# Performance work log

Measured on AMD Instinct MI355X. Metric: run time of the kernel, lower is better.

The kernel has to match this reference:

```python
import jax, jax.numpy as jnp
import numpy as np

B = 2
G = 256            # bev grid size per axis at this stride
STRIDE = 2
PAD = 2
EMB = 128
NPF = 64           # num_pos_feats = emb_dim // 2
LR = np.array([-51.2, -51.2, -3.0, 51.2, 51.2, 1.0], np.float32)
VS = np.array([0.2, 0.2], np.float32)
OFFSET = -128      # round(lr_min / (voxel * stride))
SQRT_DIM = float(np.sqrt(EMB))
Q = 65536
V = B * G * G


def pos2posemb2d(pos, num_pos_feats=NPF, temperature=10000.0):
    # standard interleaved sin/cos 2d position embedding (y first, then x)
    pos = pos * (2.0 * np.pi)
    dim_t = jnp.arange(num_pos_feats, dtype=jnp.float32)
    dim_t = temperature ** (2.0 * (dim_t // 2) / num_pos_feats)
    px = pos[..., 0:1] / dim_t
    py = pos[..., 1:2] / dim_t
    px = jnp.stack((jnp.sin(px[..., 0::2]), jnp.cos(px[..., 1::2])), axis=-1).reshape(pos.shape[0], -1)
    py = jnp.stack((jnp.sin(py[..., 0::2]), jnp.cos(py[..., 1::2])), axis=-1).reshape(pos.shape[0], -1)
    return jnp.concatenate((py, px), axis=-1)


def mlp(x, w1, b1, w2, b2):
    return jax.nn.relu(x @ w1 + b1) @ w2 + b2


def setup_inputs():
    key = jax.random.key(0)
    ks = jax.random.split(key, 16)
    # dense BEV grid of value centers -> value_map scatter is collision-free
    idx = jnp.arange(V)
    b = idx // (G * G)
    x = (idx % (G * G)) // G
    y = idx % G
    ctr_coor = jnp.stack([b, (x - 128) * STRIDE, (y - 128) * STRIDE], axis=-1).astype(jnp.int32)
    ctr_feat = jax.random.normal(ks[0], (V, EMB), jnp.float32)
    bq = jax.random.randint(ks[1], (Q,), 0, B).astype(jnp.float32)
    xy = jax.random.uniform(ks[2], (Q, 2), jnp.float32, -51.0, 51.0)
    ref_pts = jnp.concatenate([bq[:, None], xy], axis=1)
    s = 0.02
    p = lambda k, sh: jax.random.normal(k, sh, jnp.float32) * s
    return dict(
        ref_pts=ref_pts, ctr_coor=ctr_coor, ctr_feat=ctr_feat,
        q_w1=p(ks[3], (EMB, 2 * EMB)), q_b1=jnp.zeros((2 * EMB,), jnp.float32),
        q_w2=p(ks[4], (2 * EMB, EMB)), q_b2=jnp.zeros((EMB,), jnp.float32),
        v_w1=p(ks[5], (EMB, 2 * EMB)), v_b1=jnp.zeros((2 * EMB,), jnp.float32),
        v_w2=p(ks[6], (2 * EMB, EMB)), v_b2=jnp.zeros((EMB,), jnp.float32),
        se_wr=p(ks[7], (EMB, EMB)), se_br=jnp.zeros((EMB,), jnp.float32),
        se_we=p(ks[8], (EMB, EMB)), se_be=jnp.zeros((EMB,), jnp.float32),
    )


def _forward(ref_pts, ctr_feat, q_w1, q_b1, q_w2, q_b2, v_w1, v_b1, v_w2, v_b2,
             se_wr, se_br, se_we, se_be, ctr_coor):
    nv = ctr_feat.shape[0]
    lr = jnp.asarray(LR)
    vs = jnp.asarray(VS)
    # indices2metric: voxel center positions in meters
    ctr_xy = (ctr_coor[:, 1:].astype(jnp.float32) + 0.5) * vs
    # coor_to_indices: grid indices at current stride
    ctr_inds = ctr_coor[:, 1:] // STRIDE - OFFSET                 # (V,2) in [0,G)
    ref_coor = jnp.floor(ref_pts[:, 1:] / vs)                     # metric2indices
    ref_inds = (ref_coor / STRIDE - OFFSET).astype(jnp.int32)     # (Q,2) in [0,G)
    # normalized positions in [0,1]
    qp = (ref_pts[:, 1:] - lr[0:2]) / (lr[3:5] - lr[0:2])
    vp = (ctr_xy - lr[0:2]) / (lr[3:5] - lr[0:2])
    qpos = mlp(pos2posemb2d(qp), q_w1, q_b1, q_w2, q_b2)          # (Q,d)
    vpos = mlp(pos2posemb2d(vp), v_w1, v_b1, v_w2, v_b2)          # (V,d)
    # SELayer_Linear: gate value pos-emb by features
    gate = jax.nn.sigmoid(jax.nn.relu(ctr_feat @ se_wr + se_br) @ se_we + se_be)
    vpos = vpos * gate
    # build padded index map and gather 3x3 neighborhoods
    vmap_grid = -jnp.ones((B, G + 2 * PAD, G + 2 * PAD), jnp.int32)
    vmap_grid = vmap_grid.at[ctr_coor[:, 0], ctr_inds[:, 0] + PAD, ctr_inds[:, 1] + PAD].set(
        jnp.arange(nv, dtype=jnp.int32))
    r = jnp.arange(-1, 2)
    nbrs = jnp.stack(jnp.meshgrid(r, r, indexing='ij'), axis=-1).reshape(-1, 2)  # (9,2)
    bq = ref_pts[:, 0].astype(jnp.int32)
    nx = ref_inds[:, 0:1] + PAD + nbrs[:, 0]                      # (Q,9)
    ny = ref_inds[:, 1:2] + PAD + nbrs[:, 1]
    v_idx = vmap_grid[bq[:, None], nx, ny] + 1                    # missing -> 0 (padded zero row)
    vpos_pad = jnp.concatenate([jnp.zeros((1, EMB), vpos.dtype), vpos], axis=0)
    feat_pad = jnp.concatenate([jnp.zeros((1, EMB), ctr_feat.dtype), ctr_feat], axis=0)
    score = jnp.einsum('qd,qnd->qn', qpos, vpos_pad[v_idx]) / SQRT_DIM
    attn = jax.nn.softmax(score, axis=-1)
    return jnp.einsum('qn,qnd->qd', attn, feat_pad[v_idx])       # (Q,d)


def reference(ref_pts, ctr_coor, ctr_feat, q_w1, q_b1, q_w2, q_b2,
              v_w1, v_b1, v_w2, v_b2, se_wr, se_br, se_we, se_be):
    return _forward(ref_pts, ctr_feat, q_w1, q_b1, q_w2, q_b2,
                    v_w1, v_b1, v_w2, v_b2, se_wr, se_br, se_we, se_be, ctr_coor)
```

## Files before the change

### kernel.cpp

```cpp
#include <hip/hip_runtime.h>
#include <math.h>

#define SCALE_INV_SQRT_D 0.08838834764831844f

#define NQ 65536
#define NV 131072
#define NBKT 2048

typedef __attribute__((ext_vector_type(8))) short s16x8;
typedef __attribute__((ext_vector_type(4))) float f32x4;

__device__ __forceinline__ unsigned short f2bf(float f) {
    unsigned int u = __builtin_bit_cast(unsigned int, f);
    u += 0x7fffu + ((u >> 16) & 1u);
    return (unsigned short)(u >> 16);
}
__device__ __forceinline__ float bf2f(unsigned short s) {
    return __builtin_bit_cast(float, (unsigned)s << 16);
}
#define LGKM0() asm volatile("s_waitcnt lgkmcnt(0)" ::: "memory")
#define SBAR0() __builtin_amdgcn_sched_barrier(0)

__device__ __forceinline__ int kperm(int kk) {
    int i = kk & 7, gg = (kk >> 3) & 3, ks = kk >> 5;
    return (ks << 5) + ((i & 4) << 2) + (gg << 2) + (i & 3);
}

__global__ __launch_bounds__(256) void prep_kernel(
    const float* __restrict__ qw1, const float* __restrict__ qw2,
    const float* __restrict__ vw1, const float* __restrict__ vw2,
    const float* __restrict__ sewr, const float* __restrict__ sewe,
    unsigned short* __restrict__ wbuf)
{
    int i = blockIdx.x * 256 + threadIdx.x;
    float v;
    if (i < 32768)        { int li = i;          int n = li >> 7, k = li & 127;          v = qw1[k * 256 + n]; }
    else if (i < 65536)   { int li = i - 32768;  int n = li >> 8, k = kperm(li & 255);   v = qw2[k * 128 + n]; }
    else if (i < 98304)   { int li = i - 65536;  int n = li >> 7, k = li & 127;          v = vw1[k * 256 + n]; }
    else if (i < 131072)  { int li = i - 98304;  int n = li >> 8, k = kperm(li & 255);   v = vw2[k * 128 + n]; }
    else if (i < 147456)  { int li = i - 131072; int n = li >> 7, k = li & 127;          v = sewr[k * 128 + n]; }
    else                  { int li = i - 147456; int n = li >> 7, k = kperm(li & 127);   v = sewe[k * 128 + n]; }
    wbuf[i] = f2bf(v);
}

__global__ __launch_bounds__(256) void sort_zero_kernel(int* __restrict__ counts) {
    counts[blockIdx.x * 256 + threadIdx.x] = 0;
}

__global__ __launch_bounds__(256) void sort_count_kernel(
    const float* __restrict__ ref_pts, int* __restrict__ counts,
    unsigned short* __restrict__ qb)
{
    int qi = blockIdx.x * 256 + threadIdx.x;
    int b = (int)ref_pts[qi * 3 + 0];
    float x = ref_pts[qi * 3 + 1], y = ref_pts[qi * 3 + 2];
    int xi = (int)(floorf(x * 5.0f) * 0.5f + 128.0f);
    int yi = (int)(floorf(y * 5.0f) * 0.5f + 128.0f);
    int bucket = (b << 10) | ((xi >> 3) << 5) | (yi >> 3);
    qb[qi] = (unsigned short)bucket;
    atomicAdd(&counts[bucket], 1);
}

__global__ __launch_bounds__(1024) void sort_scan_kernel(
    const int* __restrict__ counts, int* __restrict__ offs)
{
    __shared__ int a[NBKT], b[NBKT];
    const int t = threadIdx.x;
    int c0 = counts[t], c1 = counts[t + 1024];
    a[t] = c0; a[t + 1024] = c1;
    __syncthreads();
    int* src = a; int* dst = b;
    for (int d = 1; d < NBKT; d <<= 1) {
        dst[t]        = src[t]        + ((t >= d)        ? src[t - d]        : 0);
        dst[t + 1024] = src[t + 1024] + ((t + 1024 >= d) ? src[t + 1024 - d] : 0);
        __syncthreads();
        int* tmp = src; src = dst; dst = tmp;
    }
    offs[t]        = src[t] - c0;
    offs[t + 1024] = src[t + 1024] - c1;
}

__global__ __launch_bounds__(256) void sort_scatter_kernel(
    const unsigned short* __restrict__ qb, int* __restrict__ offs,
    int* __restrict__ perm)
{
    int qi = blockIdx.x * 256 + threadIdx.x;
    int pos = atomicAdd(&offs[qb[qi]], 1);
    perm[pos] = qi;
}

__global__ __launch_bounds__(512, 4) void se_gate_kernel(
    const float* __restrict__ ctr_feat,
    const unsigned short* __restrict__ sewrt,
    const float* __restrict__ sebr,
    const unsigned short* __restrict__ sewetp,
    const float* __restrict__ sebe,
    unsigned short* __restrict__ gate_p,
    unsigned short* __restrict__ featb)
{
    __shared__ __attribute__((aligned(16))) char s_w[65536];
    const int t = threadIdx.x;
    for (int c = t; c < 4096; c += 512) {
        int b  = c * 16;
        int lb = b & 32767;
        int row = lb >> 8;
        int dst = (b & 32768) + (lb ^ ((row & 7) << 4));
        const unsigned short* src = (b < 32768) ? (sewrt + lb / 2) : (sewetp + (lb / 2));
        *(s16x8*)(s_w + dst) = *(const s16x8*)src;
    }
    __syncthreads();

    const int lane = t & 63, wid = t >> 6;
    const int r16 = lane & 15, g = lane >> 4;
    const int swz = (r16 & 7) << 4;
    const int w  = blockIdx.x * 8 + wid;
    const int s0 = w * 32;

    s16x8 fb[2][4];
    #pragma unroll
    for (int gr = 0; gr < 2; ++gr) {
        const int samp = s0 + gr * 16 + r16;
        #pragma unroll
        for (int ks = 0; ks < 4; ++ks) {
            const float* src = ctr_feat + (size_t)samp * 128 + ks * 32 + g * 8;
            f32x4 v0 = *(const f32x4*)(src);
            f32x4 v1 = *(const f32x4*)(src + 4);
            s16x8 pk;
            #pragma unroll
            for (int e = 0; e < 4; ++e) {
                pk[e]     = (short)f2bf(v0[e]);
                pk[4 + e] = (short)f2bf(v1[e]);
            }
            fb[gr][ks] = pk;
            *(s16x8*)(featb + (size_t)samp * 128 + ks * 32 + g * 8) = pk;
        }
    }
    s16x8 ga[2][4];
    #pragma unroll
    for (int u = 0; u < 4; ++u) {
        f32x4 a0[2], a1[2];
        #pragma unroll
        for (int gr = 0; gr < 2; ++gr) { a0[gr] = (f32x4)0.f; a1[gr] = (f32x4)0.f; }
        #pragma unroll
        for (int ks = 0; ks < 4; ++ks) {
            s16x8 w0 = *(const s16x8*)(s_w + ((((2 * u) * 16 + r16) * 256 + ks * 64 + g * 16) ^ swz));
            s16x8 w1 = *(const s16x8*)(s_w + ((((2 * u + 1) * 16 + r16) * 256 + ks * 64 + g * 16) ^ swz));
            #pragma unroll
            for (int gr = 0; gr < 2; ++gr) {
                a0[gr] = __builtin_amdgcn_mfma_f32_16x16x32_bf16(w0, fb[gr][ks], a0[gr], 0, 0, 0);
                a1[gr] = __builtin_amdgcn_mfma_f32_16x16x32_bf16(w1, fb[gr][ks], a1[gr], 0, 0, 0);
            }
        }
        f32x4 bb0 = *(const f32x4*)(sebr + 32 * u + g * 4);
        f32x4 bb1 = *(const f32x4*)(sebr + 32 * u + 16 + g * 4);
        #pragma unroll
        for (int gr = 0; gr < 2; ++gr) {
            s16x8 pk;
            #pragma unroll
            for (int r = 0; r < 4; ++r) {
                pk[r]     = (short)f2bf(fmaxf(a0[gr][r] + bb0[r], 0.f));
                pk[4 + r] = (short)f2bf(fmaxf(a1[gr][r] + bb1[r], 0.f));
            }
            ga[gr][u] = pk;
        }
    }
    #pragma unroll
    for (int n = 0; n < 8; ++n) {
        f32x4 acc[2] = {(f32x4)0.f, (f32x4)0.f};
        #pragma unroll
        for (int u = 0; u < 4; ++u) {
            s16x8 b = *(const s16x8*)(s_w + 32768 + (((n * 16 + r16) * 256 + u * 64 + g * 16) ^ swz));
            #pragma unroll
            for (int gr = 0; gr < 2; ++gr)
                acc[gr] = __builtin_amdgcn_mfma_f32_16x16x32_bf16(ga[gr][u], b, acc[gr], 0, 0, 0);
        }
        const int col = n * 16 + r16;
        const float bev = sebe[col];
        #pragma unroll
        for (int gr = 0; gr < 2; ++gr) {
            unsigned short pk[4];
            #pragma unroll
            for (int r = 0; r < 4; ++r)
                pk[r] = f2bf(1.0f / (1.0f + __expf(-(acc[gr][r] + bev))));
            *(unsigned long long*)(gate_p + (size_t)(2 * w + gr) * 2048 + col * 16 + g * 4)
                = *(const unsigned long long*)pk;
        }
    }
}

template<bool GATE>
__global__ __launch_bounds__(512, 2) void pe_mlp_kernel(
    const float* __restrict__ ref_pts,
    const int*   __restrict__ ctr_coor,
    const unsigned short* __restrict__ w1t,
    const float* __restrict__ b1,
    const unsigned short* __restrict__ w2tp,
    const float* __restrict__ b2,
    const unsigned short* __restrict__ gate_p,
    unsigned short* __restrict__ outb,
    int ntile32)
{
    __shared__ __attribute__((aligned(16))) char s_w[131072 + 32768];
    const int t = threadIdx.x;
    for (int c = t; c < 8192; c += 512) {
        int b = c * 16;
        if (b < 65536) {
            int row = b >> 8;
            *(s16x8*)(s_w + (b ^ ((row & 7) << 4))) = *(const s16x8*)(w1t + b / 2);
        } else {
            int lb = b - 65536;
            int row = lb >> 9;
            *(s16x8*)(s_w + 65536 + (lb ^ ((row & 7) << 4))) = *(const s16x8*)(w2tp + lb / 2);
        }
    }
    __syncthreads();

    const int lane = t & 63, wid = t >> 6;
    const int r16 = lane & 15, g = lane >> 4;
    const int swz = (r16 & 7) << 4;
    char* s_out = s_w + 131072 + wid * 4096;

    float b2v[8];
    #pragma unroll
    for (int n = 0; n < 8; ++n) b2v[n] = b2[n * 16 + r16];

    for (int w = blockIdx.x * 8 + wid; w < ntile32; w += gridDim.x * 8) {
        const int s0 = w * 32;

        s16x8 ape[2][4];
        #pragma unroll
        for (int gr = 0; gr < 2; ++gr) {
            const int samp = s0 + gr * 16 + r16;
            float xx, yy;
            if (GATE) {
                xx = ((float)ctr_coor[samp * 3 + 1] + 0.5f) * 0.2f;
                yy = ((float)ctr_coor[samp * 3 + 2] + 0.5f) * 0.2f;
            } else {
                xx = ref_pts[samp * 3 + 1];
                yy = ref_pts[samp * 3 + 2];
            }
            const float pnx = (xx + 51.2f) * (1.0f / 102.4f);
            const float pny = (yy + 51.2f) * (1.0f / 102.4f);
            #pragma unroll
            for (int ks = 0; ks < 4; ++ks) {
                const float p = (ks < 2) ? pny : pnx;
                s16x8 pk;
                #pragma unroll
                for (int j = 0; j < 4; ++j) {
                    float fr  = (float)(ks * 16 + g * 4 + j);
                    float rev = p * __builtin_exp2f(fr * -0.41524101186092029f);
                    float sn, cs;
                    asm("v_sin_f32 %0, %1" : "=v"(sn) : "v"(rev));
                    asm("v_cos_f32 %0, %1" : "=v"(cs) : "v"(rev));
                    pk[2 * j]     = (short)f2bf(sn);
                    pk[2 * j + 1] = (short)f2bf(cs);
                }
                ape[gr][ks] = pk;
            }
        }

        s16x8 ha[2][8];
        #pragma unroll
        for (int u = 0; u < 8; ++u) {
            f32x4 a0[2], a1[2];
            #pragma unroll
            for (int gr = 0; gr < 2; ++gr) { a0[gr] = (f32x4)0.f; a1[gr] = (f32x4)0.f; }
            #pragma unroll
            for (int ks = 0; ks < 4; ++ks) {
                s16x8 w0 = *(const s16x8*)(s_w + ((((2 * u) * 16 + r16) * 256 + ks * 64 + g * 16) ^ swz));
                s16x8 w1 = *(const s16x8*)(s_w + ((((2 * u + 1) * 16 + r16) * 256 + ks * 64 + g * 16) ^ swz));
                #pragma unroll
                for (int gr = 0; gr < 2; ++gr) {
                    a0[gr] = __builtin_amdgcn_mfma_f32_16x16x32_bf16(w0, ape[gr][ks], a0[gr], 0, 0, 0);
                    a1[gr] = __builtin_amdgcn_mfma_f32_16x16x32_bf16(w1, ape[gr][ks], a1[gr], 0, 0, 0);
                }
            }
            f32x4 bb0 = *(const f32x4*)(b1 + 32 * u + g * 4);
            f32x4 bb1 = *(const f32x4*)(b1 + 32 * u + 16 + g * 4);
            #pragma unroll
            for (int gr = 0; gr < 2; ++gr) {
                s16x8 pk;
                #pragma unroll
                for (int r = 0; r < 4; ++r) {
                    pk[r]     = (short)f2bf(fmaxf(a0[gr][r] + bb0[r], 0.f));
                    pk[4 + r] = (short)f2bf(fmaxf(a1[gr][r] + bb1[r], 0.f));
                }
                ha[gr][u] = pk;
            }
        }

        #pragma unroll
        for (int gr = 0; gr < 2; ++gr) {
            unsigned long long gk[8];
            if (GATE) {
                #pragma unroll
                for (int n = 0; n < 8; ++n)
                    gk[n] = *(const unsigned long long*)(
                        gate_p + (size_t)(2 * w + gr) * 2048 + (n * 16 + r16) * 16 + g * 4);
            }
            #pragma unroll
            for (int n = 0; n < 8; ++n) {
                f32x4 c = (f32x4)0.f;
                #pragma unroll
                for (int u = 0; u < 8; ++u) {
                    s16x8 b = *(const s16x8*)(s_w + 65536 + (((n * 16 + r16) * 512 + u * 64 + g * 16) ^ swz));
                    c = __builtin_amdgcn_mfma_f32_16x16x32_bf16(ha[gr][u], b, c, 0, 0, 0);
                }
                #pragma unroll
                for (int r = 0; r < 4; ++r) {
                    float v = c[r] + b2v[n];
                    if (GATE) v *= bf2f((unsigned short)(gk[n] >> (16 * r)));
                    *(unsigned short*)(s_out + (g * 4 + r) * 256 + ((n * 32 + r16 * 2) ^ (g << 5)))
                        = f2bf(v);
                }
            }
            LGKM0(); SBAR0();
            #pragma unroll
            for (int it = 0; it < 4; ++it) {
                int row = it * 4 + (lane >> 4);
                int cb  = (lane & 15) * 16;
                s16x8 val = *(const s16x8*)(s_out + row * 256 + (cb ^ (((row >> 2) & 3) << 5)));
                *(s16x8*)((char*)outb + (size_t)(s0 + gr * 16 + row) * 256 + cb) = val;
            }
            LGKM0(); SBAR0();
        }
    }
}

__global__ __launch_bounds__(256) void attn_kernel(
    const float* __restrict__ ref_pts,
    const int* __restrict__ perm,
    const unsigned short* __restrict__ qpos,
    const unsigned short* __restrict__ vposg,
    const unsigned short* __restrict__ featb,
    float* __restrict__ out)
{
    const int lane = threadIdx.x & 63;
    const int qi   = perm[blockIdx.x * 4 + (threadIdx.x >> 6)];

    const int   b = (int)ref_pts[qi * 3 + 0];
    const float x = ref_pts[qi * 3 + 1];
    const float y = ref_pts[qi * 3 + 2];
    const int xi = (int)(floorf(x * 5.0f) * 0.5f + 128.0f);
    const int yi = (int)(floorf(y * 5.0f) * 0.5f + 128.0f);

    const unsigned qp = *(const unsigned*)(qpos + (size_t)qi * 128 + lane * 2);
    const float qx = bf2f((unsigned short)(qp & 0xffffu));
    const float qy = bf2f((unsigned short)(qp >> 16));

    float  sc[9];
    float2 fv[9];
    #pragma unroll
    for (int n = 0; n < 9; ++n) {
        const int nx = xi + n / 3 - 1;
        const int ny = yi + n % 3 - 1;
        const bool valid = ((unsigned)nx < 256u) && ((unsigned)ny < 256u);
        float  s = 0.f;
        float2 f = {0.f, 0.f};
        if (valid) {
            const int idx = (b << 16) + (nx << 8) + ny;
            const unsigned vp = *(const unsigned*)(vposg + (size_t)idx * 128 + lane * 2);
            const unsigned fp = *(const unsigned*)(featb + (size_t)idx * 128 + lane * 2);
            f.x = bf2f((unsigned short)(fp & 0xffffu));
            f.y = bf2f((unsigned short)(fp >> 16));
            s = qx * bf2f((unsigned short)(vp & 0xffffu)) + qy * bf2f((unsigned short)(vp >> 16));
        }
        sc[n] = s;
        fv[n] = f;
    }

    #pragma unroll
    for (int off = 32; off > 0; off >>= 1) {
        #pragma unroll
        for (int n = 0; n < 9; ++n)
            sc[n] += __shfl_xor(sc[n], off, 64);
    }

    float m = -1e30f;
    #pragma unroll
    for (int n = 0; n < 9; ++n) {
        sc[n] *= SCALE_INV_SQRT_D;
        m = fmaxf(m, sc[n]);
    }
    float e[9], denom = 0.f;
    #pragma unroll
    for (int n = 0; n < 9; ++n) {
        e[n] = __expf(sc[n] - m);
        denom += e[n];
    }
    const float inv = 1.0f / denom;

    float2 o = {0.f, 0.f};
    #pragma unroll
    for (int n = 0; n < 9; ++n) {
        const float w = e[n] * inv;
        o.x += w * fv[n].x;
        o.y += w * fv[n].y;
    }
    *(float2*)(out + (size_t)qi * 128 + lane * 2) = o;
}

extern "C" void kernel_launch(void* const* d_in, const int* in_sizes, int n_in,
                              void* d_out, int out_size, void* d_ws, size_t ws_size,
                              hipStream_t stream) {
    const float* ref_pts  = (const float*)d_in[0];
    const int*   ctr_coor = (const int*)d_in[1];
    const float* ctr_feat = (const float*)d_in[2];
    const float* q_w1 = (const float*)d_in[3];
    const float* q_b1 = (const float*)d_in[4];
    const float* q_w2 = (const float*)d_in[5];
    const float* q_b2 = (const float*)d_in[6];
    const float* v_w1 = (const float*)d_in[7];
    const float* v_b1 = (const float*)d_in[8];
    const float* v_w2 = (const float*)d_in[9];
    const float* v_b2 = (const float*)d_in[10];
    const float* se_wr = (const float*)d_in[11];
    const float* se_br = (const float*)d_in[12];
    const float* se_we = (const float*)d_in[13];
    const float* se_be = (const float*)d_in[14];

    unsigned short* wbuf   = (unsigned short*)d_ws;
    unsigned short* vposg  = wbuf + 163840;
    unsigned short* qposb  = vposg + (size_t)NV * 128;
    unsigned short* gate_p = qposb + (size_t)NQ * 128;
    unsigned short* featb  = gate_p + (size_t)NV * 128;
    int*            counts = (int*)(featb + (size_t)NV * 128);
    int*            perm   = counts + NBKT;
    unsigned short* qb     = (unsigned short*)(perm + NQ);

    const unsigned short* qw1t   = wbuf;
    const unsigned short* qw2tp  = wbuf + 32768;
    const unsigned short* vw1t   = wbuf + 65536;
    const unsigned short* vw2tp  = wbuf + 98304;
    const unsigned short* sewrt  = wbuf + 131072;
    const unsigned short* sewetp = wbuf + 147456;

    prep_kernel<<<640, 256, 0, stream>>>(q_w1, q_w2, v_w1, v_w2, se_wr, se_we, wbuf);

    sort_zero_kernel<<<NBKT / 256, 256, 0, stream>>>(counts);
    sort_count_kernel<<<NQ / 256, 256, 0, stream>>>(ref_pts, counts, qb);
    sort_scan_kernel<<<1, 1024, 0, stream>>>(counts, counts);
    sort_scatter_kernel<<<NQ / 256, 256, 0, stream>>>(qb, counts, perm);

    se_gate_kernel<<<512, 512, 0, stream>>>(
        ctr_feat, sewrt, se_br, sewetp, se_be, gate_p, featb);

    pe_mlp_kernel<false><<<256, 512, 0, stream>>>(
        ref_pts, nullptr, qw1t, q_b1, qw2tp, q_b2, nullptr, qposb, NQ / 32);

    pe_mlp_kernel<true><<<256, 512, 0, stream>>>(
        nullptr, ctr_coor, vw1t, v_b1, vw2tp, v_b2, gate_p, vposg, NV / 32);

    attn_kernel<<<NQ / 4, 256, 0, stream>>>(
        ref_pts, perm, qposb, vposg, featb, (float*)d_out);
}
```

Baseline: 223.4 us.

## Process one 16-row group at a time in MLP kernel and refine LDS swizzle

Restructures the MLP tile loop so the positional embedding, first layer and second layer run per 16-sample group inside a non-unrolled loop, instead of computing both groups' embeddings and hidden activations up front. This roughly halves the live register footprint (ape/ha arrays) to raise occupancy or avoid spills, at the cost of reloading the first-layer weight fragments from LDS once per group instead of sharing them across both groups. It also changes the output staging XOR swizzle to include the row index, to reduce LDS bank conflicts on the scattered bf16 stores.

```diff
diff --git a/kernel.cpp b/kernel.cpp
--- a/kernel.cpp
+++ b/kernel.cpp
@@ -227,70 +227,61 @@
     for (int w = blockIdx.x * 8 + wid; w < ntile32; w += gridDim.x * 8) {
         const int s0 = w * 32;
 
-        s16x8 ape[2][4];
-        #pragma unroll
+        #pragma unroll 1
         for (int gr = 0; gr < 2; ++gr) {
-            const int samp = s0 + gr * 16 + r16;
-            float xx, yy;
-            if (GATE) {
-                xx = ((float)ctr_coor[samp * 3 + 1] + 0.5f) * 0.2f;
-                yy = ((float)ctr_coor[samp * 3 + 2] + 0.5f) * 0.2f;
-            } else {
-                xx = ref_pts[samp * 3 + 1];
-                yy = ref_pts[samp * 3 + 2];
-            }
-            const float pnx = (xx + 51.2f) * (1.0f / 102.4f);
-            const float pny = (yy + 51.2f) * (1.0f / 102.4f);
-            #pragma unroll
-            for (int ks = 0; ks < 4; ++ks) {
-                const float p = (ks < 2) ? pny : pnx;
+            s16x8 ape[4];
+            {
+                const int samp = s0 + gr * 16 + r16;
+                float xx, yy;
+                if (GATE) {
+                    xx = ((float)ctr_coor[samp * 3 + 1] + 0.5f) * 0.2f;
+                    yy = ((float)ctr_coor[samp * 3 + 2] + 0.5f) * 0.2f;
+                } else {
+                    xx = ref_pts[samp * 3 + 1];
+                    yy = ref_pts[samp * 3 + 2];
+                }
+                const float pnx = (xx + 51.2f) * (1.0f / 102.4f);
+                const float pny = (yy + 51.2f) * (1.0f / 102.4f);
+                #pragma unroll
+                for (int ks = 0; ks < 4; ++ks) {
+                    const float p = (ks < 2) ? pny : pnx;
+                    s16x8 pk;
+                    #pragma unroll
+                    for (int j = 0; j < 4; ++j) {
+                        float fr  = (float)(ks * 16 + g * 4 + j);
+                        float rev = p * __builtin_exp2f(fr * -0.41524101186092029f);
+                        float sn, cs;
+                        asm("v_sin_f32 %0, %1" : "=v"(sn) : "v"(rev));
+                        asm("v_cos_f32 %0, %1" : "=v"(cs) : "v"(rev));
+                        pk[2 * j]     = (short)f2bf(sn);
+                        pk[2 * j + 1] = (short)f2bf(cs);
+                    }
+                    ape[ks] = pk;
+                }
+            }
+
+            s16x8 ha[8];
+            #pragma unroll
+            for (int u = 0; u < 8; ++u) {
+                f32x4 a0 = (f32x4)0.f, a1 = (f32x4)0.f;
+                #pragma unroll
+                for (int ks = 0; ks < 4; ++ks) {
+                    s16x8 w0 = *(const s16x8*)(s_w + ((((2 * u) * 16 + r16) * 256 + ks * 64 + g * 16) ^ swz));
+                    s16x8 w1 = *(const s16x8*)(s_w + ((((2 * u + 1) * 16 + r16) * 256 + ks * 64 + g * 16) ^ swz));
+                    a0 = __builtin_amdgcn_mfma_f32_16x16x32_bf16(w0, ape[ks], a0, 0, 0, 0);
+                    a1 = __builtin_amdgcn_mfma_f32_16x16x32_bf16(w1, ape[ks], a1, 0, 0, 0);
+                }
+                f32x4 bb0 = *(const f32x4*)(b1 + 32 * u + g * 4);
+                f32x4 bb1 = *(const f32x4*)(b1 + 32 * u + 16 + g * 4);
                 s16x8 pk;
                 #pragma unroll
-                for (int j = 0; j < 4; ++j) {
-                    float fr  = (float)(ks * 16 + g * 4 + j);
-                    float rev = p * __builtin_exp2f(fr * -0.41524101186092029f);
-                    float sn, cs;
-                    asm("v_sin_f32 %0, %1" : "=v"(sn) : "v"(rev));
-                    asm("v_cos_f32 %0, %1" : "=v"(cs) : "v"(rev));
-                    pk[2 * j]     = (short)f2bf(sn);
-                    pk[2 * j + 1] = (short)f2bf(cs);
-                }
-                ape[gr][ks] = pk;
-            }
-        }
-
-        s16x8 ha[2][8];
-        #pragma unroll
-        for (int u = 0; u < 8; ++u) {
-            f32x4 a0[2], a1[2];
-            #pragma unroll
-            for (int gr = 0; gr < 2; ++gr) { a0[gr] = (f32x4)0.f; a1[gr] = (f32x4)0.f; }
-            #pragma unroll
-            for (int ks = 0; ks < 4; ++ks) {
-                s16x8 w0 = *(const s16x8*)(s_w + ((((2 * u) * 16 + r16) * 256 + ks * 64 + g * 16) ^ swz));
-                s16x8 w1 = *(const s16x8*)(s_w + ((((2 * u + 1) * 16 + r16) * 256 + ks * 64 + g * 16) ^ swz));
-                #pragma unroll
-                for (int gr = 0; gr < 2; ++gr) {
-                    a0[gr] = __builtin_amdgcn_mfma_f32_16x16x32_bf16(w0, ape[gr][ks], a0[gr], 0, 0, 0);
-                    a1[gr] = __builtin_amdgcn_mfma_f32_16x16x32_bf16(w1, ape[gr][ks], a1[gr], 0, 0, 0);
-                }
-            }
-            f32x4 bb0 = *(const f32x4*)(b1 + 32 * u + g * 4);
-            f32x4 bb1 = *(const f32x4*)(b1 + 32 * u + 16 + g * 4);
-            #pragma unroll
-            for (int gr = 0; gr < 2; ++gr) {
-                s16x8 pk;
-                #pragma unroll
                 for (int r = 0; r < 4; ++r) {
-                    pk[r]     = (short)f2bf(fmaxf(a0[gr][r] + bb0[r], 0.f));
-                    pk[4 + r] = (short)f2bf(fmaxf(a1[gr][r] + bb1[r], 0.f));
-                }
-                ha[gr][u] = pk;
-            }
-        }
-
-        #pragma unroll
-        for (int gr = 0; gr < 2; ++gr) {
+                    pk[r]     = (short)f2bf(fmaxf(a0[r] + bb0[r], 0.f));
+                    pk[4 + r] = (short)f2bf(fmaxf(a1[r] + bb1[r], 0.f));
+                }
+                ha[u] = pk;
+            }
+
             unsigned long long gk[8];
             if (GATE) {
                 #pragma unroll
@@ -298,20 +289,21 @@
                     gk[n] = *(const unsigned long long*)(
                         gate_p + (size_t)(2 * w + gr) * 2048 + (n * 16 + r16) * 16 + g * 4);
             }
+
             #pragma unroll
             for (int n = 0; n < 8; ++n) {
                 f32x4 c = (f32x4)0.f;
                 #pragma unroll
                 for (int u = 0; u < 8; ++u) {
                     s16x8 b = *(const s16x8*)(s_w + 65536 + (((n * 16 + r16) * 512 + u * 64 + g * 16) ^ swz));
-                    c = __builtin_amdgcn_mfma_f32_16x16x32_bf16(ha[gr][u], b, c, 0, 0, 0);
+                    c = __builtin_amdgcn_mfma_f32_16x16x32_bf16(ha[u], b, c, 0, 0, 0);
                 }
                 #pragma unroll
                 for (int r = 0; r < 4; ++r) {
                     float v = c[r] + b2v[n];
                     if (GATE) v *= bf2f((unsigned short)(gk[n] >> (16 * r)));
-                    *(unsigned short*)(s_out + (g * 4 + r) * 256 + ((n * 32 + r16 * 2) ^ (g << 5)))
-                        = f2bf(v);
+                    *(unsigned short*)(s_out + (g * 4 + r) * 256 +
+                        ((n * 32 + r16 * 2) ^ (((g ^ r) & 3) << 5))) = f2bf(v);
                 }
             }
             LGKM0(); SBAR0();
@@ -319,7 +311,8 @@
             for (int it = 0; it < 4; ++it) {
                 int row = it * 4 + (lane >> 4);
                 int cb  = (lane & 15) * 16;
-                s16x8 val = *(const s16x8*)(s_out + row * 256 + (cb ^ (((row >> 2) & 3) << 5)));
+                int key = (((row >> 2) ^ row) & 3) << 5;
+                s16x8 val = *(const s16x8*)(s_out + row * 256 + (cb ^ key));
                 *(s16x8*)((char*)outb + (size_t)(s0 + gr * 16 + row) * 256 + cb) = val;
             }
             LGKM0(); SBAR0();
```

New measurement: 208.5 us. 1.07x faster.
